# Kernel optimization log

Measured on AMD Instinct MI355X. Metric: run time of the kernel, lower is better.

## Reference

```python
import jax, jax.numpy as jnp
import numpy as np

L_LAYERS = 3
N_EGO = 1024
N_EDGE = 49152
M_MODES = 6
HID = 256
N_HEADS = 8
LN_EPS = 1e-5


def _layernorm(x, w, b):
    mu = jnp.mean(x, axis=-1, keepdims=True)
    var = jnp.var(x, axis=-1, keepdims=True)
    return (x - mu) * jax.lax.rsqrt(var + LN_EPS) * w + b


def setup_inputs() -> dict:
    key = jax.random.key(0)
    ks = jax.random.split(key, 16)
    f32 = jnp.float32
    H, Hh, L = HID, HID // 2, L_LAYERS

    def p(k, shape, s=0.02):
        return jax.random.normal(k, shape, f32) * s

    inp = {
        "batch": jnp.sort(jax.random.randint(ks[0], (N_EDGE,), 0, N_EGO)),
        "ego_feature": jax.random.normal(ks[1], (N_EGO, M_MODES, H), f32),
        "edge_feat": jax.random.normal(ks[2], (N_EDGE, M_MODES, Hh), f32),
        "node_feat": jax.random.normal(ks[3], (N_EDGE, M_MODES, Hh), f32),
        # stacked per-layer params
        "Wk": p(ks[4], (L, Hh, H)), "bk": jnp.zeros((L, H), f32),
        "Wq": p(ks[5], (L, H, H)), "bq": jnp.zeros((L, H), f32),
        "Wv1": p(ks[6], (L, Hh, H)), "bv1": jnp.zeros((L, H), f32),
        "Wv2": p(ks[7], (L, Hh, H)), "bv2": jnp.zeros((L, H), f32),
        "ln1_w": jnp.ones((L, H), f32), "ln1_b": jnp.zeros((L, H), f32),
        "ln2_w": jnp.ones((L, H), f32), "ln2_b": jnp.zeros((L, H), f32),
        "W1": p(ks[8], (L, H, H)), "b1": jnp.zeros((L, H), f32),
        "W2": p(ks[9], (L, H, H)), "b2": jnp.zeros((L, H), f32),
        "Wd": p(ks[10], (L, H, H)), "bd": jnp.zeros((L, H), f32),
    }
    return inp


def reference(batch, ego_feature, edge_feat, node_feat,
              Wk, bk, Wq, bq, Wv1, bv1, Wv2, bv2,
              ln1_w, ln1_b, ln2_w, ln2_b, W1, b1, W2, b2, Wd, bd):
    N, M, H = ego_feature.shape
    E = edge_feat.shape[0]
    h = N_HEADS
    dh = H // h
    L = Wk.shape[0]

    ego = ego_feature
    for i in range(L):
        # --- self-attention block (edge gather -> segment softmax -> scatter sum) ---
        xn = _layernorm(ego, ln1_w[i], ln1_b[i])                 # [N,M,H]
        k = (edge_feat @ Wk[i] + bk[i]).reshape(E, M, h, dh)     # [E,M,h,dh]
        q = (xn @ Wq[i] + bq[i]).reshape(N, M, h, dh)            # [N,M,h,dh]
        v = (edge_feat @ Wv1[i] + bv1[i]
             + node_feat @ Wv2[i] + bv2[i]).reshape(E, M, h, dh)
        scores = jnp.sum(k * q[batch], axis=-1)                  # [E,M,h]
        # segment softmax over edges grouped by ego index
        mx = jax.ops.segment_max(scores, batch, num_segments=N)  # [N,M,h]
        e = jnp.exp(scores - mx[batch])
        denom = jax.ops.segment_sum(e, batch, num_segments=N)
        alpha = e / (denom[batch] + 1e-16)                       # [E,M,h]
        agg = jax.ops.segment_sum((v * alpha[..., None]).reshape(E, M, H),
                                  batch, num_segments=N)         # [N,M,H]
        ego = ego + agg
        # --- ff block (note: 'dropout' in the original is actually a Linear) ---
        yn = _layernorm(ego, ln2_w[i], ln2_b[i])
        hmid = jax.nn.relu(yn @ W1[i] + b1[i])
        hmid = hmid @ Wd[i] + bd[i]
        ego = ego + (hmid @ W2[i] + b2[i])
    return ego
```

## Files before the change

kernel.cpp:

```cpp
#include <hip/hip_runtime.h>
#include <hip/hip_bf16.h>

#define L_LAYERS 3
#define N_EGO    1024
#define N_EDGE   49152
#define M_MODES  6
#define HID      256
#define HH       128
#define NH       8
#define DH       32
#define LN_EPS   1e-5f
#define ESS      (M_MODES * 129)
#define TE       8
#define FR       8
#define AST      129

using bf16 = __hip_bfloat16;

__device__ __forceinline__ float cvt(float x) { return x; }
__device__ __forceinline__ float cvt(bf16 x)  { return __bfloat162float(x); }
__device__ __forceinline__ float b2f(unsigned s) {
    union { float f; unsigned u; } x; x.u = s << 16; return x.f;
}

template <typename T>
__device__ __forceinline__ float ldv(const void* p, size_t i) {
    return cvt(((const T*)p)[i]);
}

template <typename T>
__device__ __forceinline__ void ld8(const void* p, size_t i, float* o);
template <>
__device__ __forceinline__ void ld8<bf16>(const void* p, size_t i, float* o) {
    uint4 u = *(const uint4*)((const bf16*)p + i);
    o[0] = b2f(u.x & 0xffffu); o[1] = b2f(u.x >> 16);
    o[2] = b2f(u.y & 0xffffu); o[3] = b2f(u.y >> 16);
    o[4] = b2f(u.z & 0xffffu); o[5] = b2f(u.z >> 16);
    o[6] = b2f(u.w & 0xffffu); o[7] = b2f(u.w >> 16);
}
template <>
__device__ __forceinline__ void ld8<float>(const void* p, size_t i, float* o) {
    const float4* q = (const float4*)((const float*)p + i);
    float4 a = q[0], b = q[1];
    o[0] = a.x; o[1] = a.y; o[2] = a.z; o[3] = a.w;
    o[4] = b.x; o[5] = b.y; o[6] = b.z; o[7] = b.w;
}

__device__ __forceinline__ void blk_sum2(float a, float b, float* red,
                                         float* oa, float* ob) {
    #pragma unroll
    for (int off = 32; off > 0; off >>= 1) {
        a += __shfl_down(a, off);
        b += __shfl_down(b, off);
    }
    int w = threadIdx.x >> 6;
    if ((threadIdx.x & 63) == 0) { red[w * 2] = a; red[w * 2 + 1] = b; }
    __syncthreads();
    *oa = red[0] + red[2] + red[4] + red[6];
    *ob = red[1] + red[3] + red[5] + red[7];
    __syncthreads();
}

__global__ void offsets_kernel(const int* __restrict__ batch, int* __restrict__ offs,
                               const void* __restrict__ ln1w, int* __restrict__ flag) {
    int n = blockIdx.x * blockDim.x + threadIdx.x;
    if (n == 0) {
        const unsigned short* u = (const unsigned short*)ln1w;
        flag[0] = (u[0] == 0x3F80 && u[1] == 0x3F80) ? 0 : 1;
    }
    if (n > N_EGO) return;
    int lo = 0, hi = N_EDGE;
    while (lo < hi) {
        int mid = (lo + hi) >> 1;
        if (batch[mid] < n) lo = mid + 1; else hi = mid;
    }
    offs[n] = lo;
}

template <typename T>
__device__ void init_body(const void* src, float* dst) {
    int i = blockIdx.x * 256 + threadIdx.x;
    dst[i] = ldv<T>(src, i);
}
__global__ void init_kernel(const void* __restrict__ src, float* __restrict__ dst,
                            const int* __restrict__ flag) {
    if (flag[0]) init_body<float>(src, dst); else init_body<bf16>(src, dst);
}

template <typename T>
__device__ void wkt_body(const void* Wk, float* WkT) {
    int idx = blockIdx.x * 256 + threadIdx.x;
    int l   = idx / (HH * HID);
    int rem = idx - l * (HH * HID);
    int j   = rem >> 8;
    int cc  = rem & (HID - 1);
    WkT[(size_t)l * HID * HH + (size_t)cc * HH + j] = ldv<T>(Wk, idx);
}
__global__ void wkt_kernel(const void* __restrict__ Wk, float* __restrict__ WkT,
                           const int* __restrict__ flag) {
    if (flag[0]) wkt_body<float>(Wk, WkT); else wkt_body<bf16>(Wk, WkT);
}

template <typename T>
__device__ void prep_body(const float* ego, const float* WkT, const void* bk,
                          const void* Wq, const void* bq, const void* lnw,
                          const void* lnb, int layer,
                          bf16* qk, float* qb) {
    extern __shared__ float sm[];
    float* xn_s = sm;
    float* q_s  = sm + 1536;
    float* red  = sm + 3072;
    int n = blockIdx.x, c = threadIdx.x;
    size_t vo = (size_t)layer * HID;

    float lw = ldv<T>(lnw, vo + c), lb = ldv<T>(lnb, vo + c);
    for (int m = 0; m < M_MODES; m++) {
        float x = ego[((size_t)n * M_MODES + m) * HID + c];
        float s1, s2;
        blk_sum2(x, x * x, red, &s1, &s2);
        float mu  = s1 * (1.0f / HID);
        float var = s2 * (1.0f / HID) - mu * mu;
        xn_s[m * HID + c] = (x - mu) * rsqrtf(fmaxf(var, 0.f) + LN_EPS) * lw + lb;
    }
    __syncthreads();

    {
        size_t wo = (size_t)layer * HID * HID;
        int co = (c & 31) * 8, mg = c >> 5;
        if (mg < M_MODES) {
            float acc[8], wv[8];
            ld8<T>(bq, vo + co, acc);
            #pragma unroll 4
            for (int k = 0; k < HID; k++) {
                ld8<T>(Wq, wo + (size_t)k * HID + co, wv);
                float x = xn_s[mg * HID + k];
                #pragma unroll
                for (int i = 0; i < 8; i++) acc[i] += x * wv[i];
            }
            #pragma unroll
            for (int i = 0; i < 8; i++) q_s[mg * HID + co + i] = acc[i];
        }
    }
    __syncthreads();

    {
        const float* WT = WkT + (size_t)layer * HID * HH;
        int j = c & (HH - 1), hg = c >> 7;
        #pragma unroll
        for (int hh = 0; hh < NH / 2; hh++) {
            int h = hg * (NH / 2) + hh;
            float a[M_MODES];
            #pragma unroll
            for (int m = 0; m < M_MODES; m++) a[m] = 0.f;
            for (int u = 0; u < DH; u++) {
                float w = WT[(size_t)(h * DH + u) * HH + j];
                #pragma unroll
                for (int m = 0; m < M_MODES; m++)
                    a[m] += q_s[m * HID + h * DH + u] * w;
            }
            #pragma unroll
            for (int m = 0; m < M_MODES; m++)
                qk[((size_t)n * 48 + m * NH + h) * HH + j] = __float2bfloat16(a[m]);
        }
        if (c < M_MODES * NH) {
            int m = c >> 3, h = c & 7;
            float s = 0.f;
            for (int u = 0; u < DH; u++)
                s += ldv<T>(bk, vo + h * DH + u) * q_s[m * HID + h * DH + u];
            qb[n * 48 + c] = s;
        }
    }
}
__global__ void prep_kernel(const float* __restrict__ ego, const float* __restrict__ WkT,
                            const void* __restrict__ bk, const void* __restrict__ Wq,
                            const void* __restrict__ bq, const void* __restrict__ lnw,
                            const void* __restrict__ lnb, int layer,
                            bf16* __restrict__ qk, float* __restrict__ qb,
                            const int* __restrict__ flag) {
    if (flag[0]) prep_body<float>(ego, WkT, bk, Wq, bq, lnw, lnb, layer, qk, qb);
    else         prep_body<bf16 >(ego, WkT, bk, Wq, bq, lnw, lnb, layer, qk, qb);
}

template <typename T>
__device__ void score_body(const void* ef, const bf16* qk, const float* qb,
                           const int* batch, bf16* scores) {
    extern __shared__ float es[];
    int c = threadIdx.x;
    int e0 = blockIdx.x * TE;

    if constexpr (sizeof(T) == 2) {
        const uint4* src = (const uint4*)((const char*)ef + (size_t)e0 * (M_MODES * HH) * 2);
        #pragma unroll
        for (int it = 0; it < 3; it++) {
            int v = it * 256 + c;
            uint4 u = src[v];
            int eo = v / 96, r = v - eo * 96, m = r >> 4, j = (r & 15) * 8;
            float* d = es + eo * ESS + m * 129 + j;
            d[0] = b2f(u.x & 0xffffu); d[1] = b2f(u.x >> 16);
            d[2] = b2f(u.y & 0xffffu); d[3] = b2f(u.y >> 16);
            d[4] = b2f(u.z & 0xffffu); d[5] = b2f(u.z >> 16);
            d[6] = b2f(u.w & 0xffffu); d[7] = b2f(u.w >> 16);
        }
    } else {
        const float4* src = (const float4*)((const char*)ef + (size_t)e0 * (M_MODES * HH) * 4);
        #pragma unroll
        for (int it = 0; it < 6; it++) {
            int v = it * 256 + c;
            float4 u = src[v];
            int eo = v / 192, r = v - eo * 192, m = r >> 5, j = (r & 31) * 4;
            float* d = es + eo * ESS + m * 129 + j;
            d[0] = u.x; d[1] = u.y; d[2] = u.z; d[3] = u.w;
        }
    }
    __syncthreads();

    int g = c & 63, w = c >> 6;
    if (g < M_MODES * NH) {
        #pragma unroll
        for (int sub = 0; sub < TE / 4; sub++) {
            int eo = sub * 4 + w, e = e0 + eo;
            int b = batch[e];
            const uint4* qrow = (const uint4*)(qk + ((size_t)b * 48 + g) * HH);
            const float* ep = es + eo * ESS + (g >> 3) * 129;
            float acc = qb[b * 48 + g];
            #pragma unroll
            for (int v = 0; v < 16; v++) {
                uint4 u = qrow[v];
                const float* e8 = ep + v * 8;
                acc += e8[0] * b2f(u.x & 0xffffu) + e8[1] * b2f(u.x >> 16)
                     + e8[2] * b2f(u.y & 0xffffu) + e8[3] * b2f(u.y >> 16)
                     + e8[4] * b2f(u.z & 0xffffu) + e8[5] * b2f(u.z >> 16)
                     + e8[6] * b2f(u.w & 0xffffu) + e8[7] * b2f(u.w >> 16);
            }
            scores[(size_t)e * 48 + g] = __float2bfloat16(acc);
        }
    }
}
__global__ void score_kernel(const void* __restrict__ ef, const bf16* __restrict__ qk,
                             const float* __restrict__ qb, const int* __restrict__ batch,
                             bf16* __restrict__ scores, const int* __restrict__ flag) {
    if (flag[0]) score_body<float>(ef, qk, qb, batch, scores);
    else         score_body<bf16 >(ef, qk, qb, batch, scores);
}

__global__ void softmax_kernel(bf16* __restrict__ scores, const int* __restrict__ offs) {
    __shared__ float red[4][48];
    int n = blockIdx.x;
    int s0 = offs[n], t1 = offs[n + 1];
    if (s0 >= t1) return;
    int c = threadIdx.x, g = c & 63, w = c >> 6;
    bool act = g < M_MODES * NH;
    float mx = -INFINITY;
    if (act) {
        for (int e = s0 + w; e < t1; e += 4)
            mx = fmaxf(mx, cvt(scores[(size_t)e * 48 + g]));
        red[w][g] = mx;
    }
    __syncthreads();
    if (act) {
        mx = fmaxf(fmaxf(red[0][g], red[1][g]), fmaxf(red[2][g], red[3][g]));
        if (!(mx == mx)) mx = 0.f;
    }
    __syncthreads();
    float den = 0.f;
    if (act) {
        for (int e = s0 + w; e < t1; e += 4) {
            float v = expf(fminf(cvt(scores[(size_t)e * 48 + g]) - mx, 0.f));
            scores[(size_t)e * 48 + g] = __float2bfloat16(v);
            den += v;
        }
        red[w][g] = den;
    }
    __syncthreads();
    if (act) {
        den = red[0][g] + red[1][g] + red[2][g] + red[3][g];
        float inv = 1.0f / (den + 1e-16f);
        for (int e = s0 + w; e < t1; e += 4)
            scores[(size_t)e * 48 + g] =
                __float2bfloat16(cvt(scores[(size_t)e * 48 + g]) * inv);
    }
}

template <typename T>
__device__ void agg_body(const void* ef, const void* nf,
                         const void* Wv1, const void* bv1,
                         const void* Wv2, const void* bv2, int layer,
                         const bf16* alpha, const int* offs, float* ego) {
    constexpr int TILE = (sizeof(T) == 2) ? 16 : 8;
    extern __shared__ float sm[];
    float* A    = sm;
    T*     stage = (T*)sm;
    float* alf  = sm + 6192;
    float* Ssum = sm + 6960;
    int n = blockIdx.x, c = threadIdx.x, part = blockIdx.y;
    int s0 = offs[n], t1 = offs[n + 1];
    if (s0 >= t1) return;
    size_t vo = (size_t)layer * HID;
    int mh = c >> 7, j = c & (HH - 1);
    const T* src = (const T*)(part ? nf : ef);

    float acc[24];
    #pragma unroll
    for (int i = 0; i < 24; i++) acc[i] = 0.f;
    float sa = 0.f;

    for (int e0 = s0; e0 < t1; e0 += TILE) {
        int cnt = t1 - e0; if (cnt > TILE) cnt = TILE;
        __syncthreads();
        for (int idx = c; idx < cnt * 48; idx += 256)
            alf[idx] = cvt(alpha[(size_t)e0 * 48 + idx]);
        {
            const uint4* s4 = (const uint4*)(src + (size_t)e0 * (M_MODES * HH));
            uint4* d4 = (uint4*)stage;
            int nv = cnt * (M_MODES * HH * (int)sizeof(T) / 16);
            for (int i = c; i < nv; i += 256) d4[i] = s4[i];
        }
        __syncthreads();
        for (int ee = 0; ee < cnt; ee++) {
            const float4* ap = (const float4*)(alf + ee * 48);
            #pragma unroll
            for (int mm = 0; mm < 3; mm++) {
                int m = mh * 3 + mm;
                float val = cvt(stage[ee * (M_MODES * HH) + m * HH + j]);
                float4 a0 = ap[m * 2 + 0];
                float4 a1 = ap[m * 2 + 1];
                acc[mm*8+0] += a0.x * val; acc[mm*8+1] += a0.y * val;
                acc[mm*8+2] += a0.z * val; acc[mm*8+3] += a0.w * val;
                acc[mm*8+4] += a1.x * val; acc[mm*8+5] += a1.y * val;
                acc[mm*8+6] += a1.z * val; acc[mm*8+7] += a1.w * val;
            }
        }
        if (c < 48)
            for (int ee = 0; ee < cnt; ee++) sa += alf[ee * 48 + c];
    }
    __syncthreads();
    #pragma unroll
    for (int mm = 0; mm < 3; mm++)
        #pragma unroll
        for (int hh = 0; hh < 8; hh++)
            A[((mh * 3 + mm) * 8 + hh) * AST + j] = acc[mm * 8 + hh];
    if (c < 48) Ssum[c] = sa;
    __syncthreads();

    size_t wo = (size_t)layer * HH * HID;
    const void* Wv = part ? Wv2 : Wv1;
    const void* bv = part ? bv2 : bv1;
    int h = c >> 5;
    float bb = ldv<T>(bv, vo + c);
    float out[M_MODES];
    #pragma unroll
    for (int m = 0; m < M_MODES; m++) out[m] = bb * Ssum[m * NH + h];
    for (int jj = 0; jj < HH; jj++) {
        float w = ldv<T>(Wv, wo + (size_t)jj * HID + c);
        #pragma unroll
        for (int m = 0; m < M_MODES; m++)
            out[m] += A[(m * NH + h) * AST + jj] * w;
    }
    #pragma unroll
    for (int m = 0; m < M_MODES; m++)
        atomicAdd(&ego[((size_t)n * M_MODES + m) * HID + c], out[m]);
}
__global__ void agg_kernel(const void* __restrict__ ef, const void* __restrict__ nf,
                           const void* __restrict__ Wv1, const void* __restrict__ bv1,
                           const void* __restrict__ Wv2, const void* __restrict__ bv2,
                           int layer, const bf16* __restrict__ alpha,
                           const int* __restrict__ offs, float* __restrict__ ego,
                           const int* __restrict__ flag) {
    if (flag[0]) agg_body<float>(ef, nf, Wv1, bv1, Wv2, bv2, layer, alpha, offs, ego);
    else         agg_body<bf16 >(ef, nf, Wv1, bv1, Wv2, bv2, layer, alpha, offs, ego);
}

template <typename T>
__device__ void ffn_body(float* ego, const void* lnw, const void* lnb,
                         const void* W1, const void* b1, const void* Wd, const void* bd,
                         const void* W2, const void* b2, int layer) {
    extern __shared__ float sm[];
    float* xs  = sm;
    float* hs  = sm + 2048;
    float* x0s = sm + 4096;
    float* red = sm + 6144;
    int r0 = blockIdx.x * FR, c = threadIdx.x;
    size_t wo = (size_t)layer * HID * HID, vo = (size_t)layer * HID;

    float lw = ldv<T>(lnw, vo + c), lb = ldv<T>(lnb, vo + c);
    for (int r = 0; r < FR; r++) {
        float x = ego[(size_t)(r0 + r) * HID + c];
        x0s[r * HID + c] = x;
        float s1, s2;
        blk_sum2(x, x * x, red, &s1, &s2);
        float mu  = s1 * (1.0f / HID);
        float var = s2 * (1.0f / HID) - mu * mu;
        xs[r * HID + c] = (x - mu) * rsqrtf(fmaxf(var, 0.f) + LN_EPS) * lw + lb;
    }
    __syncthreads();

    int co = (c & 31) * 8, r = c >> 5;
    float acc[8], wv[8];
    {
        ld8<T>(b1, vo + co, acc);
        #pragma unroll 4
        for (int k = 0; k < HID; k++) {
            ld8<T>(W1, wo + (size_t)k * HID + co, wv);
            float x = xs[r * HID + k];
            #pragma unroll
            for (int i = 0; i < 8; i++) acc[i] += x * wv[i];
        }
        #pragma unroll
        for (int i = 0; i < 8; i++) hs[r * HID + co + i] = fmaxf(acc[i], 0.f);
    }
    __syncthreads();
    {
        ld8<T>(bd, vo + co, acc);
        #pragma unroll 4
        for (int k = 0; k < HID; k++) {
            ld8<T>(Wd, wo + (size_t)k * HID + co, wv);
            float x = hs[r * HID + k];
            #pragma unroll
            for (int i = 0; i < 8; i++) acc[i] += x * wv[i];
        }
        #pragma unroll
        for (int i = 0; i < 8; i++) xs[r * HID + co + i] = acc[i];
    }
    __syncthreads();
    {
        ld8<T>(b2, vo + co, acc);
        #pragma unroll 4
        for (int k = 0; k < HID; k++) {
            ld8<T>(W2, wo + (size_t)k * HID + co, wv);
            float x = xs[r * HID + k];
            #pragma unroll
            for (int i = 0; i < 8; i++) acc[i] += x * wv[i];
        }
        float* eg = ego + (size_t)(r0 + r) * HID + co;
        #pragma unroll
        for (int i = 0; i < 8; i++) eg[i] = x0s[r * HID + co + i] + acc[i];
    }
}
__global__ void ffn_kernel(float* __restrict__ ego, const void* __restrict__ lnw,
                           const void* __restrict__ lnb, const void* __restrict__ W1,
                           const void* __restrict__ b1, const void* __restrict__ Wd,
                           const void* __restrict__ bd, const void* __restrict__ W2,
                           const void* __restrict__ b2, int layer,
                           const int* __restrict__ flag) {
    if (flag[0]) ffn_body<float>(ego, lnw, lnb, W1, b1, Wd, bd, W2, b2, layer);
    else         ffn_body<bf16 >(ego, lnw, lnb, W1, b1, Wd, bd, W2, b2, layer);
}

__global__ void out_kernel(const float* __restrict__ src, void* __restrict__ dst,
                           const int* __restrict__ flag) {
    int i = blockIdx.x * 256 + threadIdx.x;
    float v = src[i];
    if (flag[0]) ((float*)dst)[i] = v;
    else         ((bf16*)dst)[i] = __float2bfloat16(v);
}

extern "C" void kernel_launch(void* const* d_in, const int* in_sizes, int n_in,
                              void* d_out, int out_size, void* d_ws, size_t ws_size,
                              hipStream_t stream) {
    const int*  batch = (const int*)d_in[0];
    const void* ego_f = d_in[1];
    const void* edgef = d_in[2];
    const void* nodef = d_in[3];
    const void* Wk  = d_in[4];  const void* bk  = d_in[5];
    const void* Wq  = d_in[6];  const void* bq  = d_in[7];
    const void* Wv1 = d_in[8];  const void* bv1 = d_in[9];
    const void* Wv2 = d_in[10]; const void* bv2 = d_in[11];
    const void* ln1w = d_in[12]; const void* ln1b = d_in[13];
    const void* ln2w = d_in[14]; const void* ln2b = d_in[15];
    const void* W1  = d_in[16]; const void* b1  = d_in[17];
    const void* W2  = d_in[18]; const void* b2  = d_in[19];
    const void* Wd  = d_in[20]; const void* bd  = d_in[21];

    const size_t NMH = (size_t)N_EGO * M_MODES * HID;
    char* ws = (char*)d_ws;
    int*   flag   = (int*)ws;
    int*   offs   = flag + 1;
    float* ego_ws = (float*)(ws + 8192);
    bf16*  scores = (bf16*)(ws + 6299648);
    float* WkT    = (float*)(ws + 11018240);
    bf16*  qk_ws  = (bf16*)(ws + 11411456);
    float* qb_ws  = (float*)(ws + 23994368);

    const int ROWS = N_EGO * M_MODES;

    hipLaunchKernelGGL(offsets_kernel, dim3(5), dim3(256), 0, stream,
                       batch, offs, ln1w, flag);
    hipLaunchKernelGGL(init_kernel, dim3(ROWS), dim3(256), 0, stream,
                       ego_f, ego_ws, flag);
    hipLaunchKernelGGL(wkt_kernel, dim3(L_LAYERS * HH * HID / 256), dim3(256), 0, stream,
                       Wk, WkT, flag);

    const size_t PREP_LDS  = 3080 * 4;
    const size_t SCORE_LDS = (size_t)TE * ESS * 4;
    const size_t AGG_LDS   = 7008 * 4;
    const size_t FFN_LDS   = 6152 * 4;

    for (int i = 0; i < L_LAYERS; i++) {
        hipLaunchKernelGGL(prep_kernel, dim3(N_EGO), dim3(256), PREP_LDS, stream,
                           ego_ws, WkT, bk, Wq, bq, ln1w, ln1b, i, qk_ws, qb_ws, flag);
        hipLaunchKernelGGL(score_kernel, dim3(N_EDGE / TE), dim3(256), SCORE_LDS, stream,
                           edgef, qk_ws, qb_ws, batch, scores, flag);
        hipLaunchKernelGGL(softmax_kernel, dim3(N_EGO), dim3(256), 0, stream,
                           scores, offs);
        hipLaunchKernelGGL(agg_kernel, dim3(N_EGO, 2), dim3(256), AGG_LDS, stream,
                           edgef, nodef, Wv1, bv1, Wv2, bv2, i, scores, offs,
                           ego_ws, flag);
        hipLaunchKernelGGL(ffn_kernel, dim3(ROWS / FR), dim3(256), FFN_LDS, stream,
                           ego_ws, ln2w, ln2b, W1, b1, Wd, bd, W2, b2, i, flag);
    }

    hipLaunchKernelGGL(out_kernel, dim3(ROWS), dim3(256), 0, stream,
                       ego_ws, d_out, flag);
}
```

Baseline: 1.485 ms.

## Process 24 rows per FFN block to reuse each weight load three times

The FFN kernel now handles 24 rows per block instead of 8, with each thread accumulating three rows so every weight load from global memory feeds three rows of FMAs. LayerNorm is rewritten to use per-wave shuffle reductions with float4 loads instead of block-wide reductions. The residual is re-read from global memory rather than kept in shared memory. The aim is to cut redundant weight traffic and synchronisation, at the cost of more registers and fewer blocks (256 instead of 768), which lowers occupancy.

```diff
diff --git a/kernel.cpp b/kernel.cpp
--- a/kernel.cpp
+++ b/kernel.cpp
@@ -12,7 +12,7 @@
 #define LN_EPS   1e-5f
 #define ESS      (M_MODES * 129)
 #define TE       8
-#define FR       8
+#define FRB      24
 #define AST      129
 
 using bf16 = __hip_bfloat16;
@@ -375,65 +375,129 @@
                          const void* W1, const void* b1, const void* Wd, const void* bd,
                          const void* W2, const void* b2, int layer) {
     extern __shared__ float sm[];
-    float* xs  = sm;
-    float* hs  = sm + 2048;
-    float* x0s = sm + 4096;
-    float* red = sm + 6144;
-    int r0 = blockIdx.x * FR, c = threadIdx.x;
+    float* xs = sm;
+    float* hs = sm + FRB * HID;
+    int c = threadIdx.x;
+    int r0 = blockIdx.x * FRB;
     size_t wo = (size_t)layer * HID * HID, vo = (size_t)layer * HID;
-
-    float lw = ldv<T>(lnw, vo + c), lb = ldv<T>(lnb, vo + c);
-    for (int r = 0; r < FR; r++) {
-        float x = ego[(size_t)(r0 + r) * HID + c];
-        x0s[r * HID + c] = x;
-        float s1, s2;
-        blk_sum2(x, x * x, red, &s1, &s2);
-        float mu  = s1 * (1.0f / HID);
-        float var = s2 * (1.0f / HID) - mu * mu;
-        xs[r * HID + c] = (x - mu) * rsqrtf(fmaxf(var, 0.f) + LN_EPS) * lw + lb;
-    }
-    __syncthreads();
-
-    int co = (c & 31) * 8, r = c >> 5;
-    float acc[8], wv[8];
+    int lane = c & 63, wave = c >> 6;
+
     {
-        ld8<T>(b1, vo + co, acc);
+        float lw[4], lb[4];
+        #pragma unroll
+        for (int i = 0; i < 4; i++) {
+            lw[i] = ldv<T>(lnw, vo + lane * 4 + i);
+            lb[i] = ldv<T>(lnb, vo + lane * 4 + i);
+        }
+        for (int rr = 0; rr < 6; rr++) {
+            int r = wave * 6 + rr;
+            float4 x4 = *(const float4*)(ego + (size_t)(r0 + r) * HID + lane * 4);
+            float s1 = x4.x + x4.y + x4.z + x4.w;
+            float s2 = x4.x*x4.x + x4.y*x4.y + x4.z*x4.z + x4.w*x4.w;
+            #pragma unroll
+            for (int off = 32; off > 0; off >>= 1) {
+                s1 += __shfl_xor(s1, off);
+                s2 += __shfl_xor(s2, off);
+            }
+            float mu  = s1 * (1.0f / HID);
+            float var = s2 * (1.0f / HID) - mu * mu;
+            float rs  = rsqrtf(fmaxf(var, 0.f) + LN_EPS);
+            float4 o;
+            o.x = (x4.x - mu) * rs * lw[0] + lb[0];
+            o.y = (x4.y - mu) * rs * lw[1] + lb[1];
+            o.z = (x4.z - mu) * rs * lw[2] + lb[2];
+            o.w = (x4.w - mu) * rs * lw[3] + lb[3];
+            *(float4*)(xs + r * HID + lane * 4) = o;
+        }
+    }
+    __syncthreads();
+
+    int co = (c & 31) * 8, rg = c >> 5;
+    float acc[3][8], wv[8];
+
+    {
+        ld8<T>(b1, vo + co, wv);
+        #pragma unroll
+        for (int rr = 0; rr < 3; rr++)
+            #pragma unroll
+            for (int i = 0; i < 8; i++) acc[rr][i] = wv[i];
         #pragma unroll 4
         for (int k = 0; k < HID; k++) {
             ld8<T>(W1, wo + (size_t)k * HID + co, wv);
-            float x = xs[r * HID + k];
-            #pragma unroll
-            for (int i = 0; i < 8; i++) acc[i] += x * wv[i];
-        }
-        #pragma unroll
-        for (int i = 0; i < 8; i++) hs[r * HID + co + i] = fmaxf(acc[i], 0.f);
-    }
-    __syncthreads();
+            float x0 = xs[rg * HID + k];
+            float x1 = xs[(rg + 8) * HID + k];
+            float x2 = xs[(rg + 16) * HID + k];
+            #pragma unroll
+            for (int i = 0; i < 8; i++) {
+                acc[0][i] += x0 * wv[i];
+                acc[1][i] += x1 * wv[i];
+                acc[2][i] += x2 * wv[i];
+            }
+        }
+        #pragma unroll
+        for (int rr = 0; rr < 3; rr++)
+            #pragma unroll
+            for (int i = 0; i < 8; i++)
+                hs[(rg + rr * 8) * HID + co + i] = fmaxf(acc[rr][i], 0.f);
+    }
+    __syncthreads();
+
     {
-        ld8<T>(bd, vo + co, acc);
+        ld8<T>(bd, vo + co, wv);
+        #pragma unroll
+        for (int rr = 0; rr < 3; rr++)
+            #pragma unroll
+            for (int i = 0; i < 8; i++) acc[rr][i] = wv[i];
         #pragma unroll 4
         for (int k = 0; k < HID; k++) {
             ld8<T>(Wd, wo + (size_t)k * HID + co, wv);
-            float x = hs[r * HID + k];
-            #pragma unroll
-            for (int i = 0; i < 8; i++) acc[i] += x * wv[i];
-        }
-        #pragma unroll
-        for (int i = 0; i < 8; i++) xs[r * HID + co + i] = acc[i];
-    }
-    __syncthreads();
+            float x0 = hs[rg * HID + k];
+            float x1 = hs[(rg + 8) * HID + k];
+            float x2 = hs[(rg + 16) * HID + k];
+            #pragma unroll
+            for (int i = 0; i < 8; i++) {
+                acc[0][i] += x0 * wv[i];
+                acc[1][i] += x1 * wv[i];
+                acc[2][i] += x2 * wv[i];
+            }
+        }
+        __syncthreads();
+        #pragma unroll
+        for (int rr = 0; rr < 3; rr++)
+            #pragma unroll
+            for (int i = 0; i < 8; i++)
+                xs[(rg + rr * 8) * HID + co + i] = acc[rr][i];
+    }
+    __syncthreads();
+
     {
-        ld8<T>(b2, vo + co, acc);
+        ld8<T>(b2, vo + co, wv);
+        #pragma unroll
+        for (int rr = 0; rr < 3; rr++)
+            #pragma unroll
+            for (int i = 0; i < 8; i++) acc[rr][i] = wv[i];
         #pragma unroll 4
         for (int k = 0; k < HID; k++) {
             ld8<T>(W2, wo + (size_t)k * HID + co, wv);
-            float x = xs[r * HID + k];
-            #pragma unroll
-            for (int i = 0; i < 8; i++) acc[i] += x * wv[i];
-        }
-        float* eg = ego + (size_t)(r0 + r) * HID + co;
-        #pragma unroll
-        for (int i = 0; i < 8; i++) eg[i] = x0s[r * HID + co + i] + acc[i];
+            float x0 = xs[rg * HID + k];
+            float x1 = xs[(rg + 8) * HID + k];
+            float x2 = xs[(rg + 16) * HID + k];
+            #pragma unroll
+            for (int i = 0; i < 8; i++) {
+                acc[0][i] += x0 * wv[i];
+                acc[1][i] += x1 * wv[i];
+                acc[2][i] += x2 * wv[i];
+            }
+        }
+        #pragma unroll
+        for (int rr = 0; rr < 3; rr++) {
+            int row = rg + rr * 8;
+            float4* eg4 = (float4*)(ego + (size_t)(r0 + row) * HID + co);
+            float4 a = eg4[0], b = eg4[1];
+            a.x += acc[rr][0]; a.y += acc[rr][1]; a.z += acc[rr][2]; a.w += acc[rr][3];
+            b.x += acc[rr][4]; b.y += acc[rr][5]; b.z += acc[rr][6]; b.w += acc[rr][7];
+            eg4[0] = a; eg4[1] = b;
+        }
     }
 }
 __global__ void ffn_kernel(float* __restrict__ ego, const void* __restrict__ lnw,
@@ -493,7 +557,7 @@
     const size_t PREP_LDS  = 3080 * 4;
     const size_t SCORE_LDS = (size_t)TE * ESS * 4;
     const size_t AGG_LDS   = 7008 * 4;
-    const size_t FFN_LDS   = 6152 * 4;
+    const size_t FFN_LDS   = (size_t)2 * FRB * HID * 4;
 
     for (int i = 0; i < L_LAYERS; i++) {
         hipLaunchKernelGGL(prep_kernel, dim3(N_EGO), dim3(256), PREP_LDS, stream,
@@ -505,7 +569,7 @@
         hipLaunchKernelGGL(agg_kernel, dim3(N_EGO, 2), dim3(256), AGG_LDS, stream,
                            edgef, nodef, Wv1, bv1, Wv2, bv2, i, scores, offs,
                            ego_ws, flag);
-        hipLaunchKernelGGL(ffn_kernel, dim3(ROWS / FR), dim3(256), FFN_LDS, stream,
+        hipLaunchKernelGGL(ffn_kernel, dim3(ROWS / FRB), dim3(256), FFN_LDS, stream,
                            ego_ws, ln2w, ln2b, W1, b1, Wd, bd, W2, b2, i, flag);
     }
 
```

After: 1.402 ms. 5.6% less time.
